# Performance work log

Measured on AMD Instinct MI355X. Metric: run time of the kernel, lower is better.

The kernel has to match this reference:

```python
import jax, jax.numpy as jnp
import numpy as np

N_NODES = 50000
NODE_DIM = 256
HIDDEN = 512
N_EDGES = 500000


def setup_inputs() -> dict:
    key = jax.random.key(0)
    k1, k2, k3, k4 = jax.random.split(key, 4)
    x = jax.random.normal(k1, (N_NODES, NODE_DIM), dtype=jnp.float32)
    edge_index = jax.random.randint(k2, (2, N_EDGES), 0, N_NODES, dtype=jnp.int64)
    in_dim = 2 * NODE_DIM  # concat mode
    W1 = jax.random.normal(k3, (in_dim, HIDDEN), dtype=jnp.float32) / np.sqrt(in_dim)
    b1 = jnp.zeros((HIDDEN,), dtype=jnp.float32)
    W2 = jax.random.normal(k4, (HIDDEN, 1), dtype=jnp.float32) / np.sqrt(HIDDEN)
    b2 = jnp.zeros((1,), dtype=jnp.float32)
    return {"x": x, "edge_index": edge_index, "W1": W1, "b1": b1, "W2": W2, "b2": b2}


def reference(x, edge_index, W1, b1, W2, b2):
    row, col = edge_index[0], edge_index[1]
    # concat mode: edge_feat [E, 2*node_dim]
    edge_feat = jnp.concatenate([x[row], x[col]], axis=1)
    h = jax.nn.relu(edge_feat @ W1 + b1)  # [E, hidden]
    score = (h @ W2 + b2).squeeze(-1)     # [E]
    return score
```

## Files before the change

kernel.cpp:

```cpp
#include <hip/hip_runtime.h>
#include <hip/hip_bf16.h>

#define N_NODES  50000
#define NODE_DIM 256
#define HIDDEN   512
#define N_EDGES  500000
#define M_PAD    50048
#define NCAT     1024
#define KDIM     256
#define NB       391
#define CAP      1536
#define NSLOTS   (NB * CAP)
#define QSCALE   30.238095f
#define DSCALE   0.033070866f
#define DUMMY    0xFFFFFFFF00000000ULL
#define GEMM_BLKS (392 * 8)
#define SCAT_BLKS 512

typedef __attribute__((ext_vector_type(4))) unsigned short ushort4v;
typedef __attribute__((ext_vector_type(8))) __bf16 bf16x8;
typedef __attribute__((ext_vector_type(4))) float f32x4;
typedef __attribute__((ext_vector_type(4))) unsigned int uint4v;
typedef __attribute__((ext_vector_type(2))) unsigned int uint2v;
typedef __attribute__((ext_vector_type(2))) unsigned long long ull2;
typedef __attribute__((ext_vector_type(2))) float float2v;

__device__ __forceinline__ unsigned short f2bf(float f) {
  unsigned int u = __builtin_bit_cast(unsigned int, f);
  u += 0x7fffu + ((u >> 16) & 1u);
  return (unsigned short)(u >> 16);
}

__device__ __forceinline__ void gload16(const void* g, void* l) {
  __builtin_amdgcn_global_load_lds(
      (__attribute__((address_space(1))) void*)(g),
      (__attribute__((address_space(3))) void*)(l),
      16, 0, 0);
}

__global__ void prep_kernel(const float* __restrict__ x, unsigned short* __restrict__ xb,
                            const float* __restrict__ W1, unsigned short* __restrict__ wt,
                            int* __restrict__ counts, unsigned long long* __restrict__ slots) {
  const int b = blockIdx.x;
  if (b < 2048) {
    const int total4 = M_PAD * NODE_DIM / 4;
    const int valid4 = N_NODES * NODE_DIM / 4;
    for (int i = b * 256 + threadIdx.x; i < total4; i += 2048 * 256) {
      ushort4v o;
      if (i < valid4) {
        float4 v = ((const float4*)x)[i];
        o[0] = f2bf(v.x); o[1] = f2bf(v.y); o[2] = f2bf(v.z); o[3] = f2bf(v.w);
      } else {
        o[0] = 0; o[1] = 0; o[2] = 0; o[3] = 0;
      }
      ((ushort4v*)xb)[i] = o;
    }
  } else if (b < 3072) {
    int i = (b - 2048) * 256 + threadIdx.x;
    int n = i >> 8;
    int k = i & 255;
    int srow = (n >= HIDDEN) ? (NODE_DIM + k) : k;
    int scol = n & (HIDDEN - 1);
    wt[i] = f2bf(W1[srow * HIDDEN + scol]);
  } else if (b == 3072) {
    for (int i = threadIdx.x; i < NB; i += 256) counts[i] = 0;
  } else {
    int bb = b - 3073;
    for (int i = bb * 256 + threadIdx.x; i < NSLOTS; i += 512 * 256)
      slots[i] = DUMMY;
  }
}

__global__ __launch_bounds__(256, 2) void gemm_kernel(
    const unsigned short* __restrict__ Xb,
    const unsigned short* __restrict__ Wt,
    const float* __restrict__ b1,
    unsigned short* __restrict__ CbA,
    signed char* __restrict__ CbB,
    const int* __restrict__ ei,
    int* __restrict__ counts,
    unsigned long long* __restrict__ slots) {
  __shared__ unsigned short As[128 * 64];
  __shared__ unsigned short Bs[128 * 64];
  __shared__ int h[NB];
  __shared__ int bbase[NB];
  const int t = threadIdx.x;
  const int bid = blockIdx.x;

  if (bid >= GEMM_BLKS) {
    const int sb = bid - GEMM_BLKS;
    const int chunk = (N_EDGES + SCAT_BLKS - 1) / SCAT_BLKS;
    const int e0 = sb * chunk;
    const int e1 = min(e0 + chunk, N_EDGES);
    for (int i = t; i < NB; i += 256) h[i] = 0;
    __syncthreads();
    for (int e = e0 + t; e < e1; e += 256)
      atomicAdd(&h[ei[e] >> 7], 1);
    __syncthreads();
    for (int i = t; i < NB; i += 256) {
      int c = h[i];
      bbase[i] = c ? atomicAdd(&counts[i], c) : 0;
      h[i] = 0;
    }
    __syncthreads();
    for (int e = e0 + t; e < e1; e += 256) {
      int r = ei[e];
      int c = ei[N_EDGES + e];
      int b = r >> 7;
      int idx = bbase[b] + atomicAdd(&h[b], 1);
      slots[(size_t)b * CAP + idx] =
          (unsigned long long)r | ((unsigned long long)c << 16) | ((unsigned long long)e << 32);
    }
    return;
  }

  const int w = t >> 6;
  const int lane = t & 63;
  const int xcd = bid & 7;
  const int loc = bid >> 3;
  const int tileN = loc / 49;
  const int tileM = xcd * 49 + (loc - tileN * 49);
  if (tileM >= 391) return;
  const int wm = w >> 1, wn = w & 1;

  f32x4 acc[4][4] = {};

  const int rowA0 = tileM * 128;
  const int rowB0 = tileN * 128;
  const int rstage = t >> 3;
  const int cstage = (t & 7) * 8;

  for (int kk = 0; kk < KDIM; kk += 64) {
#pragma unroll
    for (int i = 0; i < 4; ++i) {
      const unsigned short* srcA = Xb + (size_t)(rowA0 + i * 32 + rstage) * KDIM + kk + cstage;
      gload16(srcA, (char*)As + i * 4096 + w * 1024);
      const unsigned short* srcB = Wt + (size_t)(rowB0 + i * 32 + rstage) * KDIM + kk + cstage;
      gload16(srcB, (char*)Bs + i * 4096 + w * 1024);
    }
    __syncthreads();

#pragma unroll
    for (int kk2 = 0; kk2 < 64; kk2 += 32) {
      bf16x8 a[4], bfr[4];
#pragma unroll
      for (int fm = 0; fm < 4; ++fm)
        a[fm] = *(const bf16x8*)&As[(wm * 64 + fm * 16 + (lane & 15)) * 64 + kk2 + (lane >> 4) * 8];
#pragma unroll
      for (int fn = 0; fn < 4; ++fn)
        bfr[fn] = *(const bf16x8*)&Bs[(wn * 64 + fn * 16 + (lane & 15)) * 64 + kk2 + (lane >> 4) * 8];
#pragma unroll
      for (int fm = 0; fm < 4; ++fm)
#pragma unroll
        for (int fn = 0; fn < 4; ++fn)
          acc[fm][fn] = __builtin_amdgcn_mfma_f32_16x16x32_bf16(a[fm], bfr[fn], acc[fm][fn], 0, 0, 0);
    }
    __syncthreads();
  }

  const int row0 = tileM * 128 + wm * 64;
  if (tileN < 4) {
    const int col0 = tileN * 128 + wn * 64;
    float b1v[4];
#pragma unroll
    for (int fn = 0; fn < 4; ++fn) b1v[fn] = b1[col0 + fn * 16 + (lane & 15)];
#pragma unroll
    for (int fm = 0; fm < 4; ++fm)
#pragma unroll
      for (int fn = 0; fn < 4; ++fn)
#pragma unroll
        for (int r = 0; r < 4; ++r) {
          int row = row0 + fm * 16 + (lane >> 4) * 4 + r;
          int col = col0 + fn * 16 + (lane & 15);
          CbA[(size_t)row * HIDDEN + col] = f2bf(acc[fm][fn][r] + b1v[fn]);
        }
  } else {
    const int col0 = (tileN - 4) * 128 + wn * 64;
#pragma unroll
    for (int fm = 0; fm < 4; ++fm)
#pragma unroll
      for (int fn = 0; fn < 4; ++fn)
#pragma unroll
        for (int r = 0; r < 4; ++r) {
          int row = row0 + fm * 16 + (lane >> 4) * 4 + r;
          int col = col0 + fn * 16 + (lane & 15);
          float v = fminf(fmaxf(acc[fm][fn][r], -4.2f), 4.2f);
          CbB[(size_t)row * HIDDEN + col] = (signed char)__float2int_rn(v * QSCALE);
        }
  }
}

__device__ __forceinline__ float2v edge_mlp_pk(uint4v ua, uint2v ub,
                                               const float2v* w2p) {
  const float2v dscale2 = {DSCALE, DSCALE};
  const float2v zero2 = {0.f, 0.f};
  float2v acc = zero2;
#pragma unroll
  for (int j = 0; j < 4; ++j) {
    unsigned int au = ua[j];
    float2v a;
    a[0] = __builtin_bit_cast(float, au << 16);
    a[1] = __builtin_bit_cast(float, au & 0xffff0000u);
    unsigned int ubw = ub[j >> 1];
    int sh = (j & 1) * 16;
    float2v q;
    q[0] = (float)(int)(signed char)(ubw >> sh);
    q[1] = (float)(int)(signed char)(ubw >> (sh + 8));
    float2v h = __builtin_elementwise_fma(q, dscale2, a);
    h = __builtin_elementwise_max(h, zero2);
    acc = __builtin_elementwise_fma(h, w2p[j], acc);
  }
  return acc;
}

__global__ __launch_bounds__(256) void edge_kernel(
    const unsigned short* __restrict__ CbA,
    const signed char* __restrict__ CbB,
    const unsigned long long* __restrict__ slots,
    const float* __restrict__ W2,
    const float* __restrict__ b2,
    float* __restrict__ out) {
  const int lane = threadIdx.x & 63;
  const int xcd = blockIdx.x & 7;
  const int lwid = (blockIdx.x >> 3) * 4 + (threadIdx.x >> 6);
  const int nlw = (gridDim.x >> 3) * 4;
  const int per_xcd = NSLOTS / 8;
  const int pbase = xcd * per_xcd;
  const int base = lane * 8;

  float2v w2p[4];
  {
    float4 u0 = *(const float4*)&W2[base];
    float4 u1 = *(const float4*)&W2[base + 4];
    w2p[0] = (float2v){u0.x, u0.y};
    w2p[1] = (float2v){u0.z, u0.w};
    w2p[2] = (float2v){u1.x, u1.y};
    w2p[3] = (float2v){u1.z, u1.w};
  }
  const float bias2 = b2[0];

  const int pend = pbase + per_xcd;
  for (int p = pbase + lwid * 4; p < pend; p += nlw * 4) {
    ull2 rrA = *(const ull2*)(slots + p);
    ull2 rrB = *(const ull2*)(slots + p + 2);
    const int id0 = (int)(rrA[0] >> 32);
    const int id1 = (int)(rrA[1] >> 32);
    const int id2 = (int)(rrB[0] >> 32);
    const int id3 = (int)(rrB[1] >> 32);
    if ((id0 & id1 & id2 & id3) < 0) continue;
    const int r0 = (int)(rrA[0] & 0xFFFF), c0 = (int)((rrA[0] >> 16) & 0xFFFF);
    const int r1 = (int)(rrA[1] & 0xFFFF), c1 = (int)((rrA[1] >> 16) & 0xFFFF);
    const int r2 = (int)(rrB[0] & 0xFFFF), c2 = (int)((rrB[0] >> 16) & 0xFFFF);
    const int r3 = (int)(rrB[1] & 0xFFFF), c3 = (int)((rrB[1] >> 16) & 0xFFFF);
    uint4v ua0 = *(const uint4v*)(CbA + (size_t)r0 * HIDDEN + base);
    uint2v ub0 = *(const uint2v*)(CbB + (size_t)c0 * HIDDEN + base);
    uint4v ua1 = *(const uint4v*)(CbA + (size_t)r1 * HIDDEN + base);
    uint2v ub1 = *(const uint2v*)(CbB + (size_t)c1 * HIDDEN + base);
    uint4v ua2 = *(const uint4v*)(CbA + (size_t)r2 * HIDDEN + base);
    uint2v ub2 = *(const uint2v*)(CbB + (size_t)c2 * HIDDEN + base);
    uint4v ua3 = *(const uint4v*)(CbA + (size_t)r3 * HIDDEN + base);
    uint2v ub3 = *(const uint2v*)(CbB + (size_t)c3 * HIDDEN + base);

    float2v a0 = edge_mlp_pk(ua0, ub0, w2p);
    float2v a1 = edge_mlp_pk(ua1, ub1, w2p);
    float2v a2 = edge_mlp_pk(ua2, ub2, w2p);
    float2v a3 = edge_mlp_pk(ua3, ub3, w2p);
    float acc0 = a0[0] + a0[1];
    float acc1 = a1[0] + a1[1];
    float acc2 = a2[0] + a2[1];
    float acc3 = a3[0] + a3[1];

#pragma unroll
    for (int off = 32; off >= 16; off >>= 1) {
      acc0 += __shfl_xor(acc0, off, 64);
      acc1 += __shfl_xor(acc1, off, 64);
      acc2 += __shfl_xor(acc2, off, 64);
      acc3 += __shfl_xor(acc3, off, 64);
    }
    const int q = lane >> 4;
    float v = (q == 0) ? acc0 : (q == 1) ? acc1 : (q == 2) ? acc2 : acc3;
#pragma unroll
    for (int off = 8; off; off >>= 1)
      v += __shfl_xor(v, off, 64);
    if ((lane & 15) == 0) {
      const int idq = (q == 0) ? id0 : (q == 1) ? id1 : (q == 2) ? id2 : id3;
      if (idq >= 0) out[idq] = v + bias2;
    }
  }
}

extern "C" void kernel_launch(void* const* d_in, const int* in_sizes, int n_in,
                              void* d_out, int out_size, void* d_ws, size_t ws_size,
                              hipStream_t stream) {
  const float* x  = (const float*)d_in[0];
  const int*   ei = (const int*)d_in[1];
  const float* W1 = (const float*)d_in[2];
  const float* b1 = (const float*)d_in[3];
  const float* W2 = (const float*)d_in[4];
  const float* b2 = (const float*)d_in[5];
  float* out = (float*)d_out;

  char* ws = (char*)d_ws;
  const size_t xb_bytes  = (size_t)M_PAD * KDIM * 2;
  const size_t wt_bytes  = (size_t)NCAT * KDIM * 2;
  const size_t cbA_bytes = (size_t)M_PAD * HIDDEN * 2;
  const size_t cbB_bytes = (size_t)M_PAD * HIDDEN;
  unsigned short* xb  = (unsigned short*)ws;
  unsigned short* wt  = (unsigned short*)(ws + xb_bytes);
  unsigned short* cbA = (unsigned short*)(ws + xb_bytes + wt_bytes);
  signed char*    cbB = (signed char*)(ws + xb_bytes + wt_bytes + cbA_bytes);
  char* tail = ws + xb_bytes + wt_bytes + cbA_bytes + cbB_bytes;
  int* counts = (int*)tail;
  unsigned long long* slots = (unsigned long long*)(tail + 4096);

  hipLaunchKernelGGL(prep_kernel, dim3(3585), dim3(256), 0, stream, x, xb, W1, wt, counts, slots);
  hipLaunchKernelGGL(gemm_kernel, dim3(GEMM_BLKS + SCAT_BLKS), dim3(256), 0, stream,
                     xb, wt, b1, cbA, cbB, ei, counts, slots);
  hipLaunchKernelGGL(edge_kernel, dim3(2048), dim3(256), 0, stream, cbA, cbB, slots, W2, b2, out);
}
```

Measured before the change: 137.9 us.

## Stage per-bucket CbA rows in LDS with finer 32-row edge buckets

Edges are now bucketed by row into groups of 32 nodes instead of 128, and the edge kernel launches one block per bucket. Each block first copies the 32 CbA rows for its bucket into shared memory, then reads those rows from LDS rather than gathering them at random from global memory. The loop length comes from the per-bucket count, so empty slot regions are no longer scanned. In exchange, each block uses 32KB of LDS, which limits occupancy. Per-bucket capacity is also tighter, so an unusually dense bucket could overflow its slots.

```diff
diff --git a/kernel.cpp b/kernel.cpp
--- a/kernel.cpp
+++ b/kernel.cpp
@@ -8,8 +8,8 @@
 #define M_PAD    50048
 #define NCAT     1024
 #define KDIM     256
-#define NB       391
-#define CAP      1536
+#define NB       1564
+#define CAP      448
 #define NSLOTS   (NB * CAP)
 #define QSCALE   30.238095f
 #define DSCALE   0.033070866f
@@ -95,7 +95,7 @@
     for (int i = t; i < NB; i += 256) h[i] = 0;
     __syncthreads();
     for (int e = e0 + t; e < e1; e += 256)
-      atomicAdd(&h[ei[e] >> 7], 1);
+      atomicAdd(&h[ei[e] >> 5], 1);
     __syncthreads();
     for (int i = t; i < NB; i += 256) {
       int c = h[i];
@@ -106,7 +106,7 @@
     for (int e = e0 + t; e < e1; e += 256) {
       int r = ei[e];
       int c = ei[N_EDGES + e];
-      int b = r >> 7;
+      int b = r >> 5;
       int idx = bbase[b] + atomicAdd(&h[b], 1);
       slots[(size_t)b * CAP + idx] =
           (unsigned long long)r | ((unsigned long long)c << 16) | ((unsigned long long)e << 32);
@@ -217,16 +217,25 @@
     const unsigned short* __restrict__ CbA,
     const signed char* __restrict__ CbB,
     const unsigned long long* __restrict__ slots,
+    const int* __restrict__ counts,
     const float* __restrict__ W2,
     const float* __restrict__ b2,
     float* __restrict__ out) {
-  const int lane = threadIdx.x & 63;
-  const int xcd = blockIdx.x & 7;
-  const int lwid = (blockIdx.x >> 3) * 4 + (threadIdx.x >> 6);
-  const int nlw = (gridDim.x >> 3) * 4;
-  const int per_xcd = NSLOTS / 8;
-  const int pbase = xcd * per_xcd;
+  __shared__ unsigned short Asm[32 * HIDDEN];
+  const int t = threadIdx.x;
+  const int lane = t & 63;
+  const int wid = t >> 6;
+  const int b = blockIdx.x;
   const int base = lane * 8;
+
+  {
+    const char* srcBase = (const char*)(CbA + (size_t)b * 32 * HIDDEN);
+#pragma unroll
+    for (int k = 0; k < 8; ++k) {
+      int chunk = t + k * 256;
+      gload16(srcBase + chunk * 16, (char*)Asm + chunk * 16);
+    }
+  }
 
   float2v w2p[4];
   {
@@ -238,27 +247,30 @@
     w2p[3] = (float2v){u1.z, u1.w};
   }
   const float bias2 = b2[0];
-
-  const int pend = pbase + per_xcd;
-  for (int p = pbase + lwid * 4; p < pend; p += nlw * 4) {
+  __syncthreads();
+
+  const int cnt = min(counts[b], CAP);
+  const int pbase = b * CAP;
+  const int pend = pbase + ((cnt + 3) & ~3);
+
+  for (int p = pbase + wid * 4; p < pend; p += 16) {
     ull2 rrA = *(const ull2*)(slots + p);
     ull2 rrB = *(const ull2*)(slots + p + 2);
     const int id0 = (int)(rrA[0] >> 32);
     const int id1 = (int)(rrA[1] >> 32);
     const int id2 = (int)(rrB[0] >> 32);
     const int id3 = (int)(rrB[1] >> 32);
-    if ((id0 & id1 & id2 & id3) < 0) continue;
     const int r0 = (int)(rrA[0] & 0xFFFF), c0 = (int)((rrA[0] >> 16) & 0xFFFF);
     const int r1 = (int)(rrA[1] & 0xFFFF), c1 = (int)((rrA[1] >> 16) & 0xFFFF);
     const int r2 = (int)(rrB[0] & 0xFFFF), c2 = (int)((rrB[0] >> 16) & 0xFFFF);
     const int r3 = (int)(rrB[1] & 0xFFFF), c3 = (int)((rrB[1] >> 16) & 0xFFFF);
-    uint4v ua0 = *(const uint4v*)(CbA + (size_t)r0 * HIDDEN + base);
+    uint4v ua0 = *(const uint4v*)&Asm[(r0 & 31) * HIDDEN + base];
     uint2v ub0 = *(const uint2v*)(CbB + (size_t)c0 * HIDDEN + base);
-    uint4v ua1 = *(const uint4v*)(CbA + (size_t)r1 * HIDDEN + base);
+    uint4v ua1 = *(const uint4v*)&Asm[(r1 & 31) * HIDDEN + base];
     uint2v ub1 = *(const uint2v*)(CbB + (size_t)c1 * HIDDEN + base);
-    uint4v ua2 = *(const uint4v*)(CbA + (size_t)r2 * HIDDEN + base);
+    uint4v ua2 = *(const uint4v*)&Asm[(r2 & 31) * HIDDEN + base];
     uint2v ub2 = *(const uint2v*)(CbB + (size_t)c2 * HIDDEN + base);
-    uint4v ua3 = *(const uint4v*)(CbA + (size_t)r3 * HIDDEN + base);
+    uint4v ua3 = *(const uint4v*)&Asm[(r3 & 31) * HIDDEN + base];
     uint2v ub3 = *(const uint2v*)(CbB + (size_t)c3 * HIDDEN + base);
 
     float2v a0 = edge_mlp_pk(ua0, ub0, w2p);
@@ -311,10 +323,11 @@
   signed char*    cbB = (signed char*)(ws + xb_bytes + wt_bytes + cbA_bytes);
   char* tail = ws + xb_bytes + wt_bytes + cbA_bytes + cbB_bytes;
   int* counts = (int*)tail;
-  unsigned long long* slots = (unsigned long long*)(tail + 4096);
+  unsigned long long* slots = (unsigned long long*)(tail + 8192);
 
   hipLaunchKernelGGL(prep_kernel, dim3(3585), dim3(256), 0, stream, x, xb, W1, wt, counts, slots);
   hipLaunchKernelGGL(gemm_kernel, dim3(GEMM_BLKS + SCAT_BLKS), dim3(256), 0, stream,
                      xb, wt, b1, cbA, cbB, ei, counts, slots);
-  hipLaunchKernelGGL(edge_kernel, dim3(2048), dim3(256), 0, stream, cbA, cbB, slots, W2, b2, out);
-}
+  hipLaunchKernelGGL(edge_kernel, dim3(NB), dim3(256), 0, stream,
+                     cbA, cbB, slots, counts, W2, b2, out);
+}
```

After: 136.3 us. Within noise of the previous version (-1.1%).
